# Performance work log

Measured on AMD Instinct MI355X. Metric: run time of the kernel, lower is better.

## Reference

```python
import jax, jax.numpy as jnp
import numpy as np

HEAD_DIM = 64
NUM_HEADS = 32
ROPE_BASE = 10000.0


def _rope_interleaved(x):
    # x: [B, T, H, D]; interleaved RoPE on query, seqlen_offset = 0
    B, T, H, D = x.shape
    inv_freq = 1.0 / (ROPE_BASE ** (jnp.arange(0, D, 2, dtype=jnp.float32) / D))  # [D/2]
    t = jnp.arange(T, dtype=jnp.float32)
    freqs = t[:, None] * inv_freq[None, :]          # [T, D/2]
    cos = jnp.cos(freqs)[None, :, None, :]          # [1, T, 1, D/2]
    sin = jnp.sin(freqs)[None, :, None, :]
    x1 = x[..., 0::2]
    x2 = x[..., 1::2]
    o1 = x1 * cos - x2 * sin
    o2 = x1 * sin + x2 * cos
    out = jnp.stack([o1, o2], axis=-1).reshape(x.shape)  # re-interleave
    return out


def setup_inputs() -> dict:
    key = jax.random.key(0)
    k1, k2, k3, k4, k5 = jax.random.split(key, 5)
    B, T, Dm = 2, 2048, 2048
    H, Dh = NUM_HEADS, HEAD_DIM
    scale = 0.02
    return {
        "hidden_states": jax.random.normal(k1, (B, T, Dm), jnp.float32),
        "shared_k": jax.random.normal(k2, (B, T, H, Dh), jnp.float32),
        "shared_v": jax.random.normal(k3, (B, T, H, Dh), jnp.float32),
        "Wq": jax.random.normal(k4, (Dm, Dm), jnp.float32) * scale,
        "Wo": jax.random.normal(k5, (Dm, Dm), jnp.float32) * scale,
    }


def reference(hidden_states, shared_k, shared_v, Wq, Wo):
    B, T, Dm = hidden_states.shape
    H, Dh = NUM_HEADS, HEAD_DIM
    # q projection (nn.Linear: x @ W.T)
    q = (hidden_states @ Wq.T).reshape(B, T, H, Dh)
    # rotary on q only (seqlen_offset = shared_k_len - q_len = 0)
    q = _rope_interleaved(q)
    # parallel causal attention over shared KV cache (window_size=None)
    scale = 1.0 / jnp.sqrt(jnp.asarray(Dh, jnp.float32))
    scores = jnp.einsum('bqhd,bkhd->bhqk', q, shared_k) * scale
    causal = jnp.tril(jnp.ones((T, T), dtype=bool))
    scores = jnp.where(causal[None, None], scores, -jnp.inf)
    p = jax.nn.softmax(scores, axis=-1)
    o = jnp.einsum('bhqk,bkhd->bqhd', p, shared_v)
    o = o.reshape(B, T, Dm)
    return o @ Wo.T
```

## Files before the change

kernel.cpp:

```cpp
#include <hip/hip_runtime.h>
#include <stdint.h>

typedef short short8 __attribute__((ext_vector_type(8)));
typedef float f32x4 __attribute__((ext_vector_type(4)));
typedef int int2v __attribute__((ext_vector_type(2)));
typedef int int4v __attribute__((ext_vector_type(4)));

#define QSCALE 0.1803368801111137f
#define FREQC 0.4152410118609203f

__device__ __forceinline__ float bf2f(unsigned short u) {
    union { unsigned int i; float f; } x; x.i = ((unsigned int)u) << 16; return x.f;
}
__device__ __forceinline__ unsigned short f2bf(float f) {
    union { float f; unsigned int i; } x; x.f = f;
    unsigned int i = x.i;
    unsigned int r = i + 0x7FFFu + ((i >> 16) & 1u);
    return (unsigned short)(r >> 16);
}
__device__ __forceinline__ int cvtpk_bf16(float lo, float hi) {
    int r;
    asm("v_cvt_pk_bf16_f32 %0, %1, %2" : "=v"(r) : "v"(lo), "v"(hi));
    return r;
}

#define GLDS16(g, l) \
    __builtin_amdgcn_global_load_lds((const __attribute__((address_space(1))) void*)(g), \
                                     (__attribute__((address_space(3))) void*)(l), 16, 0, 0)

#define WAITVM(n) asm volatile("s_waitcnt vmcnt(" #n ")" ::: "memory")

__global__ __launch_bounds__(256) void cvt_tr(
    const float* __restrict__ hs, const float* __restrict__ k,
    const float* __restrict__ wq, const float* __restrict__ wo,
    const float* __restrict__ V,
    unsigned short* __restrict__ hs_b, unsigned short* __restrict__ k_b,
    unsigned short* __restrict__ wq_b, unsigned short* __restrict__ wo_b,
    unsigned short* __restrict__ Vt) {
    __shared__ float s[64 * 65];
    int blk = blockIdx.x;
    int tid = threadIdx.x;
    if (blk < 12288) {
        const float* in; unsigned short* out; int i;
        if (blk < 4096)        { in = hs; out = hs_b; i = blk; }
        else if (blk < 8192)   { in = k;  out = k_b;  i = blk - 4096; }
        else if (blk < 10240)  { in = wq; out = wq_b; i = blk - 8192; }
        else                   { in = wo; out = wo_b; i = blk - 10240; }
        const float4* in4 = (const float4*)in;
        float4 v0 = in4[(size_t)i * 512 + tid];
        float4 v1 = in4[(size_t)i * 512 + 256 + tid];
        ushort4 o0, o1;
        o0.x = f2bf(v0.x); o0.y = f2bf(v0.y); o0.z = f2bf(v0.z); o0.w = f2bf(v0.w);
        o1.x = f2bf(v1.x); o1.y = f2bf(v1.y); o1.z = f2bf(v1.z); o1.w = f2bf(v1.w);
        ushort4* out4 = (ushort4*)out;
        out4[(size_t)i * 512 + tid] = o0;
        out4[(size_t)i * 512 + 256 + tid] = o1;
        return;
    }
    int tb = blk - 12288;
    int t0 = (tb & 31) * 64;
    int bh = tb >> 5;
    int b = bh >> 5, h = bh & 31;
#pragma unroll
    for (int it = 0; it < 4; ++it) {
        int c = tid + it * 256;
        int t = c >> 4;
        int d0 = (c & 15) * 4;
        float4 v = *(const float4*)(V + (size_t)(((b * 2048 + t0 + t) * 32 + h)) * 64 + d0);
        s[t * 65 + d0 + 0] = v.x; s[t * 65 + d0 + 1] = v.y;
        s[t * 65 + d0 + 2] = v.z; s[t * 65 + d0 + 3] = v.w;
    }
    __syncthreads();
#pragma unroll
    for (int it = 0; it < 2; ++it) {
        int c = tid + it * 256;
        int d = c >> 3;
        int tt = (c & 7) * 8;
        short8 pk;
#pragma unroll
        for (int j = 0; j < 8; ++j) pk[j] = (short)f2bf(s[(tt + j) * 65 + d]);
        *(short8*)(Vt + (size_t)(bh * 64 + d) * 2048 + t0 + tt) = pk;
    }
}

template <bool BF16_OUT>
__global__ __launch_bounds__(512, 2) void gemm_bt(
    const unsigned short* __restrict__ A,
    const unsigned short* __restrict__ B,
    void* __restrict__ Cout,
    int M, int N, int K)
{
    __shared__ __align__(16) unsigned short lA[3][256 * 64];
    __shared__ __align__(16) unsigned short lB[3][128 * 64];
    int tid = threadIdx.x, lane = tid & 63, wave = tid >> 6;
    int wm = (wave >> 1) * 64, wn = (wave & 1) * 64;
    int m16 = lane & 15, q = lane >> 4;
    int rowBase = blockIdx.x * 256, colBase = blockIdx.y * 128;
    f32x4 acc[4][4] = {};

    int sr = lane >> 3;
    int g  = (lane & 7) ^ sr;
    const unsigned short* gAp = A + (size_t)(rowBase + wave * 32 + sr) * K + g * 8;
    const unsigned short* gBp = B + (size_t)(colBase + wave * 16 + sr) * K + g * 8;

#define GSTAGE(buf, k0)                                                                     \
    do {                                                                                    \
        _Pragma("unroll")                                                                   \
        for (int gi = 0; gi < 4; ++gi)                                                      \
            GLDS16(gAp + (size_t)(8 * gi) * K + (k0), &lA[buf][(wave * 32 + 8 * gi) * 64]); \
        _Pragma("unroll")                                                                   \
        for (int gi = 0; gi < 2; ++gi)                                                      \
            GLDS16(gBp + (size_t)(8 * gi) * K + (k0), &lB[buf][(wave * 16 + 8 * gi) * 64]); \
    } while (0)

    GSTAGE(0, 0);
    GSTAGE(1, 64);
    WAITVM(6);
    __builtin_amdgcn_s_barrier();
    int cur = 0, nxt = 2;
    const int NT = 32;
    for (int i = 0; i < NT; ++i) {
        if (i < NT - 2) GSTAGE(nxt, (i + 2) * 64);
        if (i < NT - 2)      WAITVM(12);
        else if (i == NT - 2) WAITVM(6);
        else                  WAITVM(0);
        __builtin_amdgcn_s_barrier();
        const unsigned short* la = &lA[cur][0];
        const unsigned short* lb = &lB[cur][0];
#pragma unroll
        for (int kk = 0; kk < 2; ++kk) {
            short8 af[4], bfr[4];
#pragma unroll
            for (int i2 = 0; i2 < 4; ++i2) {
                int RA = wm + i2 * 16 + m16;
                af[i2]  = *(const short8*)&la[RA * 64 + (((kk * 4 + q) ^ (RA & 7)) * 8)];
                int RB = wn + i2 * 16 + m16;
                bfr[i2] = *(const short8*)&lb[RB * 64 + (((kk * 4 + q) ^ (RB & 7)) * 8)];
            }
#pragma unroll
            for (int i2 = 0; i2 < 4; ++i2)
#pragma unroll
                for (int jn = 0; jn < 4; ++jn)
                    acc[i2][jn] = __builtin_amdgcn_mfma_f32_16x16x32_bf16(af[i2], bfr[jn], acc[i2][jn], 0, 0, 0);
        }
        __builtin_amdgcn_s_barrier();
        cur = (cur == 2) ? 0 : cur + 1;
        nxt = (nxt == 2) ? 0 : nxt + 1;
    }
#pragma unroll
    for (int i = 0; i < 4; ++i)
#pragma unroll
        for (int jn = 0; jn < 4; ++jn)
#pragma unroll
            for (int r = 0; r < 4; ++r) {
                int row = rowBase + wm + i * 16 + q * 4 + r;
                int col = colBase + wn + jn * 16 + m16;
                float v = acc[i][jn][r];
                if (BF16_OUT) ((unsigned short*)Cout)[(size_t)row * N + col] = f2bf(v);
                else          ((float*)Cout)[(size_t)row * N + col] = v;
            }
}

__global__ __launch_bounds__(256, 4) void attn(
    const unsigned short* __restrict__ Q,
    const unsigned short* __restrict__ Kb,
    const unsigned short* __restrict__ Vt,
    unsigned short* __restrict__ O)
{
    __shared__ __align__(16) unsigned short sK[2][64 * 64];
    __shared__ __align__(16) unsigned short sV[2][64 * 64];
    int tid = threadIdx.x, lane = tid & 63, w = tid >> 6;
    int m16 = lane & 15, q = lane >> 4;
    int rx = m16 & 7;
    int flat = blockIdx.x;
    int bh = flat & 63, p = flat >> 6;
    int b = bh >> 5, h = bh & 31;
    int qtA = 31 - p, qtB = p;

    short8 aqA0, aqA1, aqB0, aqB1;
    {
        int tA = qtA * 64 + w * 16 + m16;
        int tB = qtB * 64 + w * 16 + m16;
        const unsigned short* rowA = Q + (size_t)(b * 2048 + tA) * 2048 + h * 64 + q * 8;
        const unsigned short* rowB = Q + (size_t)(b * 2048 + tB) * 2048 + h * 64 + q * 8;
        short8 a0 = *(const short8*)rowA, a1 = *(const short8*)(rowA + 32);
        short8 b0 = *(const short8*)rowB, b1 = *(const short8*)(rowB + 32);
        float tfA = (float)tA, tfB = (float)tB;
#pragma unroll
        for (int j = 0; j < 4; ++j) {
            float inv0 = __builtin_amdgcn_exp2f(-FREQC * (float)(q * 4 + j));
            float inv1 = __builtin_amdgcn_exp2f(-FREQC * (float)(16 + q * 4 + j));
            float cA0 = __cosf(tfA * inv0), sA0 = __sinf(tfA * inv0);
            float cA1 = __cosf(tfA * inv1), sA1 = __sinf(tfA * inv1);
            float cB0 = __cosf(tfB * inv0), sB0 = __sinf(tfB * inv0);
            float cB1 = __cosf(tfB * inv1), sB1 = __sinf(tfB * inv1);
            float x1, x2;
            x1 = bf2f((unsigned short)a0[2 * j]); x2 = bf2f((unsigned short)a0[2 * j + 1]);
            aqA0[2 * j]     = (short)f2bf((x1 * cA0 - x2 * sA0) * QSCALE);
            aqA0[2 * j + 1] = (short)f2bf((x1 * sA0 + x2 * cA0) * QSCALE);
            x1 = bf2f((unsigned short)a1[2 * j]); x2 = bf2f((unsigned short)a1[2 * j + 1]);
            aqA1[2 * j]     = (short)f2bf((x1 * cA1 - x2 * sA1) * QSCALE);
            aqA1[2 * j + 1] = (short)f2bf((x1 * sA1 + x2 * cA1) * QSCALE);
            x1 = bf2f((unsigned short)b0[2 * j]); x2 = bf2f((unsigned short)b0[2 * j + 1]);
            aqB0[2 * j]     = (short)f2bf((x1 * cB0 - x2 * sB0) * QSCALE);
            aqB0[2 * j + 1] = (short)f2bf((x1 * sB0 + x2 * cB0) * QSCALE);
            x1 = bf2f((unsigned short)b1[2 * j]); x2 = bf2f((unsigned short)b1[2 * j + 1]);
            aqB1[2 * j]     = (short)f2bf((x1 * cB1 - x2 * sB1) * QSCALE);
            aqB1[2 * j + 1] = (short)f2bf((x1 * sB1 + x2 * cB1) * QSCALE);
        }
    }

    float lrunA = 0.f, lrunB = 0.f;
    f32x4 accOA[4], accOB[4];
#pragma unroll
    for (int nt = 0; nt < 4; ++nt) {
        f32x4 z = {0.f, 0.f, 0.f, 0.f};
        accOA[nt] = z; accOB[nt] = z;
    }

    int sr = lane >> 3, g = (lane & 7) ^ sr;
    int rb = w * 16;
    const unsigned short* kgp = Kb + (size_t)(b * 2048 + rb + sr) * 2048 + h * 64 + g * 8;
    const unsigned short* vgp = Vt + (size_t)((b * 32 + h) * 64 + rb + sr) * 2048 + g * 8;

#define ASTAGE(kt, bi)                                                               \
    do {                                                                             \
        int kb0 = (kt) * 64;                                                         \
        _Pragma("unroll")                                                            \
        for (int gi = 0; gi < 2; ++gi) {                                             \
            GLDS16(kgp + (size_t)(kb0 + 8 * gi) * 2048, &sK[bi][(rb + 8 * gi) * 64]); \
            GLDS16(vgp + (size_t)(8 * gi) * 2048 + kb0, &sV[bi][(rb + 8 * gi) * 64]); \
        }                                                                            \
    } while (0)

    ASTAGE(0, 0);
    WAITVM(0);
    __builtin_amdgcn_s_barrier();
    int cur = 0;
    for (int kt = 0; kt <= qtA; ++kt) {
        if (kt < qtA) {
            ASTAGE(kt + 1, cur ^ 1);
            WAITVM(4);
        } else {
            WAITVM(0);
        }
        __builtin_amdgcn_s_barrier();
        bool doB = (kt <= qtB);
        bool diagA = (kt == qtA), diagB = (kt == qtB);
        const unsigned short* kbuf = sK[cur];
        const unsigned short* vbuf = sV[cur];

        int pkA[4][2], pkB[4][2];
#pragma unroll
        for (int nt = 0; nt < 4; ++nt) {
            const unsigned short* kr = kbuf + (nt * 16 + m16) * 64;
            short8 bk0 = *(const short8*)&kr[(q ^ rx) * 8];
            short8 bk1 = *(const short8*)&kr[((4 + q) ^ rx) * 8];
            f32x4 zA = {0.f, 0.f, 0.f, 0.f};
            zA = __builtin_amdgcn_mfma_f32_16x16x32_bf16(bk0, aqA0, zA, 0, 0, 0);
            zA = __builtin_amdgcn_mfma_f32_16x16x32_bf16(bk1, aqA1, zA, 0, 0, 0);
            float e[4];
#pragma unroll
            for (int r = 0; r < 4; ++r) {
                float s = zA[r];
                if (diagA && (nt * 16 + q * 4 + r > w * 16 + m16)) s = -__builtin_inff();
                e[r] = __builtin_amdgcn_exp2f(s);
            }
            lrunA += (e[0] + e[1]) + (e[2] + e[3]);
            pkA[nt][0] = cvtpk_bf16(e[0], e[1]);
            pkA[nt][1] = cvtpk_bf16(e[2], e[3]);
            if (doB) {
                f32x4 zB = {0.f, 0.f, 0.f, 0.f};
                zB = __builtin_amdgcn_mfma_f32_16x16x32_bf16(bk0, aqB0, zB, 0, 0, 0);
                zB = __builtin_amdgcn_mfma_f32_16x16x32_bf16(bk1, aqB1, zB, 0, 0, 0);
                float eb[4];
#pragma unroll
                for (int r = 0; r < 4; ++r) {
                    float s = zB[r];
                    if (diagB && (nt * 16 + q * 4 + r > w * 16 + m16)) s = -__builtin_inff();
                    eb[r] = __builtin_amdgcn_exp2f(s);
                }
                lrunB += (eb[0] + eb[1]) + (eb[2] + eb[3]);
                pkB[nt][0] = cvtpk_bf16(eb[0], eb[1]);
                pkB[nt][1] = cvtpk_bf16(eb[2], eb[3]);
            }
        }

        int4v tA0 = {pkA[0][0], pkA[0][1], pkA[1][0], pkA[1][1]};
        int4v tA1 = {pkA[2][0], pkA[2][1], pkA[3][0], pkA[3][1]};
        short8 apA0 = __builtin_bit_cast(short8, tA0);
        short8 apA1 = __builtin_bit_cast(short8, tA1);
        short8 apB0, apB1;
        if (doB) {
            int4v tB0 = {pkB[0][0], pkB[0][1], pkB[1][0], pkB[1][1]};
            int4v tB1 = {pkB[2][0], pkB[2][1], pkB[3][0], pkB[3][1]};
            apB0 = __builtin_bit_cast(short8, tB0);
            apB1 = __builtin_bit_cast(short8, tB1);
        }

#pragma unroll
        for (int nt = 0; nt < 4; ++nt) {
            const unsigned short* vr = vbuf + (nt * 16 + m16) * 64;
            int2v a0 = *(const int2v*)&vr[(((q >> 1) + 0) ^ rx) * 8 + (q & 1) * 4];
            int2v a1 = *(const int2v*)&vr[(((q >> 1) + 2) ^ rx) * 8 + (q & 1) * 4];
            int2v a2 = *(const int2v*)&vr[(((q >> 1) + 4) ^ rx) * 8 + (q & 1) * 4];
            int2v a3 = *(const int2v*)&vr[(((q >> 1) + 6) ^ rx) * 8 + (q & 1) * 4];
            int4v tv0 = {a0.x, a0.y, a1.x, a1.y};
            int4v tv1 = {a2.x, a2.y, a3.x, a3.y};
            short8 bv0 = __builtin_bit_cast(short8, tv0);
            short8 bv1 = __builtin_bit_cast(short8, tv1);
            accOA[nt] = __builtin_amdgcn_mfma_f32_16x16x32_bf16(apA0, bv0, accOA[nt], 0, 0, 0);
            accOA[nt] = __builtin_amdgcn_mfma_f32_16x16x32_bf16(apA1, bv1, accOA[nt], 0, 0, 0);
            if (doB) {
                accOB[nt] = __builtin_amdgcn_mfma_f32_16x16x32_bf16(apB0, bv0, accOB[nt], 0, 0, 0);
                accOB[nt] = __builtin_amdgcn_mfma_f32_16x16x32_bf16(apB1, bv1, accOB[nt], 0, 0, 0);
            }
        }
        __builtin_amdgcn_s_barrier();
        cur ^= 1;
    }

    lrunA += __shfl_xor(lrunA, 16); lrunA += __shfl_xor(lrunA, 32);
    lrunB += __shfl_xor(lrunB, 16); lrunB += __shfl_xor(lrunB, 32);
    float invA = 1.0f / lrunA, invB = 1.0f / lrunB;
    float nA[4], nB[4];
#pragma unroll
    for (int r = 0; r < 4; ++r) {
        nA[r] = __shfl(invA, q * 4 + r);
        nB[r] = __shfl(invB, q * 4 + r);
    }
#pragma unroll
    for (int nt = 0; nt < 4; ++nt)
#pragma unroll
        for (int r = 0; r < 4; ++r) {
            int col = h * 64 + nt * 16 + m16;
            O[(size_t)(b * 2048 + qtA * 64 + w * 16 + q * 4 + r) * 2048 + col] =
                f2bf(accOA[nt][r] * nA[r]);
            O[(size_t)(b * 2048 + qtB * 64 + w * 16 + q * 4 + r) * 2048 + col] =
                f2bf(accOB[nt][r] * nB[r]);
        }
}

extern "C" void kernel_launch(void* const* d_in, const int* in_sizes, int n_in,
                              void* d_out, int out_size, void* d_ws, size_t ws_size,
                              hipStream_t stream) {
    const float* hs = (const float*)d_in[0];
    const float* sk = (const float*)d_in[1];
    const float* sv = (const float*)d_in[2];
    const float* wq = (const float*)d_in[3];
    const float* wo = (const float*)d_in[4];
    float* out = (float*)d_out;

    char* ws = (char*)d_ws;
    unsigned short* hid_b = (unsigned short*)(ws);
    unsigned short* wq_b  = (unsigned short*)(ws + ((size_t)16 << 20));
    unsigned short* wo_b  = (unsigned short*)(ws + ((size_t)24 << 20));
    unsigned short* k_b   = (unsigned short*)(ws + ((size_t)32 << 20));
    unsigned short* vt_b  = (unsigned short*)(ws + ((size_t)48 << 20));
    unsigned short* q_b   = (unsigned short*)(ws + ((size_t)64 << 20));
    unsigned short* o_b   = (unsigned short*)(ws + ((size_t)80 << 20));

    cvt_tr<<<14336, 256, 0, stream>>>(hs, sk, wq, wo, sv, hid_b, k_b, wq_b, wo_b, vt_b);
    gemm_bt<true><<<dim3(16, 16), 512, 0, stream>>>(hid_b, wq_b, (void*)q_b, 4096, 2048, 2048);
    attn<<<1024, 256, 0, stream>>>(q_b, k_b, vt_b, o_b);
    gemm_bt<false><<<dim3(16, 16), 512, 0, stream>>>(o_b, wo_b, (void*)out, 4096, 2048, 2048);
}
```

Before: 293.2 us.

## Split GEMM k-loop into ping-pong phases and raise MFMA priority

The GEMM main loop is restructured into two half-tile phases. Each phase loads its LDS fragments, then hits a barrier and an explicit lgkmcnt wait plus sched_barrier before issuing MFMAs at elevated wave priority (s_setprio). The global-to-LDS prefetch is issued after the first fragment loads, and the vmcnt wait moves to the middle of the iteration, so memory traffic overlaps compute across waves. The attention kernel also wraps its MFMA groups in s_setprio. This adds more barriers per iteration, and the wait placement has to stay correct for the triple-buffered ring.

Measured after the change: 294.7 us. About the same (+0.5%).

```diff
diff --git a/kernel.cpp b/kernel.cpp
--- a/kernel.cpp
+++ b/kernel.cpp
@@ -29,6 +29,8 @@
                                      (__attribute__((address_space(3))) void*)(l), 16, 0, 0)
 
 #define WAITVM(n) asm volatile("s_waitcnt vmcnt(" #n ")" ::: "memory")
+#define LGKM0()   do { asm volatile("s_waitcnt lgkmcnt(0)" ::: "memory"); \
+                       __builtin_amdgcn_sched_barrier(0); } while (0)
 
 __global__ __launch_bounds__(256) void cvt_tr(
     const float* __restrict__ hs, const float* __restrict__ k,
@@ -120,29 +122,46 @@
     int cur = 0, nxt = 2;
     const int NT = 32;
     for (int i = 0; i < NT; ++i) {
-        if (i < NT - 2) GSTAGE(nxt, (i + 2) * 64);
-        if (i < NT - 2)      WAITVM(12);
-        else if (i == NT - 2) WAITVM(6);
-        else                  WAITVM(0);
-        __builtin_amdgcn_s_barrier();
         const unsigned short* la = &lA[cur][0];
         const unsigned short* lb = &lB[cur][0];
-#pragma unroll
-        for (int kk = 0; kk < 2; ++kk) {
-            short8 af[4], bfr[4];
-#pragma unroll
-            for (int i2 = 0; i2 < 4; ++i2) {
-                int RA = wm + i2 * 16 + m16;
-                af[i2]  = *(const short8*)&la[RA * 64 + (((kk * 4 + q) ^ (RA & 7)) * 8)];
-                int RB = wn + i2 * 16 + m16;
-                bfr[i2] = *(const short8*)&lb[RB * 64 + (((kk * 4 + q) ^ (RB & 7)) * 8)];
-            }
-#pragma unroll
-            for (int i2 = 0; i2 < 4; ++i2)
-#pragma unroll
-                for (int jn = 0; jn < 4; ++jn)
-                    acc[i2][jn] = __builtin_amdgcn_mfma_f32_16x16x32_bf16(af[i2], bfr[jn], acc[i2][jn], 0, 0, 0);
-        }
+        short8 af0[4], bf0[4];
+#pragma unroll
+        for (int i2 = 0; i2 < 4; ++i2) {
+            int RA = wm + i2 * 16 + m16;
+            af0[i2] = *(const short8*)&la[RA * 64 + ((q ^ (RA & 7)) * 8)];
+            int RB = wn + i2 * 16 + m16;
+            bf0[i2] = *(const short8*)&lb[RB * 64 + ((q ^ (RB & 7)) * 8)];
+        }
+        if (i < NT - 2) GSTAGE(nxt, (i + 2) * 64);
+        __builtin_amdgcn_s_barrier();
+        LGKM0();
+        __builtin_amdgcn_s_setprio(1);
+#pragma unroll
+        for (int i2 = 0; i2 < 4; ++i2)
+#pragma unroll
+            for (int jn = 0; jn < 4; ++jn)
+                acc[i2][jn] = __builtin_amdgcn_mfma_f32_16x16x32_bf16(af0[i2], bf0[jn], acc[i2][jn], 0, 0, 0);
+        __builtin_amdgcn_s_setprio(0);
+        __builtin_amdgcn_s_barrier();
+        short8 af1[4], bf1[4];
+#pragma unroll
+        for (int i2 = 0; i2 < 4; ++i2) {
+            int RA = wm + i2 * 16 + m16;
+            af1[i2] = *(const short8*)&la[RA * 64 + (((4 + q) ^ (RA & 7)) * 8)];
+            int RB = wn + i2 * 16 + m16;
+            bf1[i2] = *(const short8*)&lb[RB * 64 + (((4 + q) ^ (RB & 7)) * 8)];
+        }
+        if (i <= NT - 3) WAITVM(6);
+        else             WAITVM(0);
+        __builtin_amdgcn_s_barrier();
+        LGKM0();
+        __builtin_amdgcn_s_setprio(1);
+#pragma unroll
+        for (int i2 = 0; i2 < 4; ++i2)
+#pragma unroll
+            for (int jn = 0; jn < 4; ++jn)
+                acc[i2][jn] = __builtin_amdgcn_mfma_f32_16x16x32_bf16(af1[i2], bf1[jn], acc[i2][jn], 0, 0, 0);
+        __builtin_amdgcn_s_setprio(0);
         __builtin_amdgcn_s_barrier();
         cur = (cur == 2) ? 0 : cur + 1;
         nxt = (nxt == 2) ? 0 : nxt + 1;
@@ -257,8 +276,10 @@
             short8 bk0 = *(const short8*)&kr[(q ^ rx) * 8];
             short8 bk1 = *(const short8*)&kr[((4 + q) ^ rx) * 8];
             f32x4 zA = {0.f, 0.f, 0.f, 0.f};
+            __builtin_amdgcn_s_setprio(1);
             zA = __builtin_amdgcn_mfma_f32_16x16x32_bf16(bk0, aqA0, zA, 0, 0, 0);
             zA = __builtin_amdgcn_mfma_f32_16x16x32_bf16(bk1, aqA1, zA, 0, 0, 0);
+            __builtin_amdgcn_s_setprio(0);
             float e[4];
 #pragma unroll
             for (int r = 0; r < 4; ++r) {
@@ -271,8 +292,10 @@
             pkA[nt][1] = cvtpk_bf16(e[2], e[3]);
             if (doB) {
                 f32x4 zB = {0.f, 0.f, 0.f, 0.f};
+                __builtin_amdgcn_s_setprio(1);
                 zB = __builtin_amdgcn_mfma_f32_16x16x32_bf16(bk0, aqB0, zB, 0, 0, 0);
                 zB = __builtin_amdgcn_mfma_f32_16x16x32_bf16(bk1, aqB1, zB, 0, 0, 0);
+                __builtin_amdgcn_s_setprio(0);
                 float eb[4];
 #pragma unroll
                 for (int r = 0; r < 4; ++r) {
@@ -309,12 +332,14 @@
             int4v tv1 = {a2.x, a2.y, a3.x, a3.y};
             short8 bv0 = __builtin_bit_cast(short8, tv0);
             short8 bv1 = __builtin_bit_cast(short8, tv1);
+            __builtin_amdgcn_s_setprio(1);
             accOA[nt] = __builtin_amdgcn_mfma_f32_16x16x32_bf16(apA0, bv0, accOA[nt], 0, 0, 0);
             accOA[nt] = __builtin_amdgcn_mfma_f32_16x16x32_bf16(apA1, bv1, accOA[nt], 0, 0, 0);
             if (doB) {
                 accOB[nt] = __builtin_amdgcn_mfma_f32_16x16x32_bf16(apB0, bv0, accOB[nt], 0, 0, 0);
                 accOB[nt] = __builtin_amdgcn_mfma_f32_16x16x32_bf16(apB1, bv1, accOB[nt], 0, 0, 0);
             }
+            __builtin_amdgcn_s_setprio(0);
         }
         __builtin_amdgcn_s_barrier();
         cur ^= 1;
```
